# Optimization experiments

Measured on AMD Instinct MI355X. Metric: run time of the kernel, lower is better.

Reference implementation:

```python
import jax, jax.numpy as jnp
import numpy as np

B, S, D, U, L = 32, 8192, 64, 32, 2
VOCAB, E, NV = 10000, 500000, 50000


def _gru_dir(x, K, R, b_in, b_rec, reverse):
    # Keras GRU (v2 defaults, reset_after=True) over time axis.
    # x: [B, S, D_in]; K: [D_in, 3U]; R: [U, 3U]; b_in, b_rec: [3U]
    Bsz = x.shape[0]
    units = R.shape[0]

    def step(h, xt):
        mx = xt @ K + b_in          # [B, 3U]
        mi = h @ R + b_rec          # [B, 3U]
        xz, xr, xh = jnp.split(mx, 3, axis=-1)
        iz, ir, ih = jnp.split(mi, 3, axis=-1)
        z = jax.nn.sigmoid(xz + iz)
        r = jax.nn.sigmoid(xr + ir)
        hh = jnp.tanh(xh + r * ih)
        h = z * h + (1.0 - z) * hh
        return h, h

    h0 = jnp.zeros((Bsz, units), x.dtype)
    _, ys = jax.lax.scan(step, h0, jnp.swapaxes(x, 0, 1), reverse=reverse)
    return jnp.swapaxes(ys, 0, 1)  # [B, S, U]


def setup_inputs() -> dict:
    key = jax.random.key(0)
    ks = jax.random.split(key, 10)
    embedding_table = jax.random.normal(ks[0], (VOCAB, D), jnp.float32) * 0.02
    gru_kernels = jax.random.normal(ks[1], (L, 2, D, 3 * U), jnp.float32) * 0.1
    gru_rec_kernels = jax.random.normal(ks[2], (L, 2, U, 3 * U), jnp.float32) * 0.1
    gru_biases = jax.random.normal(ks[3], (L, 2, 2, 3 * U), jnp.float32) * 0.01
    linear_w = jax.random.normal(ks[4], (2 * U, 2 * U), jnp.float32) * 0.05
    embedding_gather_matrix = jax.random.randint(ks[5], (B, S), 0, VOCAB, jnp.int32)
    sequence_lengths = jax.random.randint(ks[6], (B,), 1, S + 1, jnp.int32)
    variable_bound_token_ids = jax.random.randint(ks[7], (E,), 0, B * S, jnp.int32)
    token_variable_ids = jax.random.randint(ks[8], (E,), 0, NV, jnp.int32)
    return {
        "embedding_table": embedding_table,
        "gru_kernels": gru_kernels,
        "gru_rec_kernels": gru_rec_kernels,
        "gru_biases": gru_biases,
        "linear_w": linear_w,
        "embedding_gather_matrix": embedding_gather_matrix,
        "sequence_lengths": sequence_lengths,
        "variable_bound_token_ids": variable_bound_token_ids,
        "token_variable_ids": token_variable_ids,
        "num_variables": NV,
    }


def reference(embedding_table, gru_kernels, gru_rec_kernels, gru_biases, linear_w,
              embedding_gather_matrix, sequence_lengths,
              variable_bound_token_ids, token_variable_ids, num_variables):
    # gather_nd: token id -> embedding, [B, S, D]
    x = embedding_table[embedding_gather_matrix]
    mask = (jnp.arange(S)[None, :, None] < sequence_lengths[:, None, None]).astype(x.dtype)

    def var_emb(cur):
        # gather per-occurrence token embeddings, unsorted_segment_mean per variable
        flat = cur.reshape(-1, cur.shape[-1])                      # [B*S, F]
        tgt = flat[variable_bound_token_ids]                       # [E, F]
        sums = jax.ops.segment_sum(tgt, token_variable_ids, num_segments=num_variables)
        cnt = jax.ops.segment_sum(jnp.ones((tgt.shape[0], 1), tgt.dtype),
                                  token_variable_ids, num_segments=num_variables)
        return sums / jnp.maximum(cnt, 1.0)                        # [NV, F]

    cur = x
    n_layers = gru_kernels.shape[0]
    for i in range(n_layers):
        cur = cur * mask
        f = _gru_dir(cur, gru_kernels[i, 0], gru_rec_kernels[i, 0],
                     gru_biases[i, 0, 0], gru_biases[i, 0, 1], reverse=False)
        b = _gru_dir(cur, gru_kernels[i, 1], gru_rec_kernels[i, 1],
                     gru_biases[i, 1, 0], gru_biases[i, 1, 1], reverse=True)
        cur = jnp.concatenate([f, b], axis=-1)                     # [B, S, 2U]
        if i < n_layers - 1:
            # consistency layer: scatter variable means back to tokens
            ve = var_emb(cur)                                      # [NV, 2U]
            per_tok = ve[token_variable_ids]                       # [E, 2U]
            upd = jnp.zeros((B * S, cur.shape[-1]), cur.dtype)
            upd = upd.at[variable_bound_token_ids].add(per_tok)    # scatter_nd (add dups)
            cur = cur + upd.reshape(B, S, -1)

    variable_embeddings = var_emb(cur)                             # [NV, 2U]
    classification_representation = variable_embeddings @ linear_w # dropout omitted (inference)
    return variable_embeddings, classification_representation
```

## Files before the change

### kernel.cpp

```cpp
#include <hip/hip_runtime.h>
#include <hip/hip_bf16.h>

typedef unsigned short ushort_t;
typedef unsigned int uint_t;

#define BB    32
#define SS    8192
#define DD    64
#define UU    32
#define GG    96
#define NEDGE 500000
#define NVAR  50000
#define VOCAB 10000

#define WT_KERN   0
#define WT_REC    24576
#define WT_BIAS   36864
#define WT_LW     37632
#define WT_TOTAL  41728

#define OFF_FLAG  0
#define OFF_WTS   16
#define OFF_SUMS  (OFF_WTS + WT_TOTAL)
#define OFF_CNT   (OFF_SUMS + NVAR*64)
#define OFF_CUR0  (OFF_CNT + NVAR)
#define OFF_CUR1  (OFF_CUR0 + BB*SS*DD)
#define WS_NEED_BYTES ((size_t)(OFF_CUR1 + BB*SS*DD) * 4)

__device__ __forceinline__ float bf2f(uint_t h) {
    union { uint_t u; float f; } v; v.u = h << 16; return v.f;
}
__device__ __forceinline__ float frcp(float x) { return __builtin_amdgcn_rcpf(x); }
__device__ __forceinline__ float sigm(float x) { return frcp(1.f + __expf(-x)); }
__device__ __forceinline__ float ftanh(float x) {
    return 1.f - 2.f * frcp(__expf(2.f * x) + 1.f);
}
__device__ __forceinline__ float fetchv(const void* p, int j, bool bf) {
    return bf ? bf2f(((const ushort_t*)p)[j]) : ((const float*)p)[j];
}

__global__ void k_sniff(const ushort_t* __restrict__ tab, int* __restrict__ flag) {
    if (threadIdx.x == 0 && blockIdx.x == 0) {
        int insane = 0;
        for (int i = 0; i < 128; i++) {
            float a = fabsf(bf2f(tab[i]));
            if (!(a <= 100.f)) insane++;
        }
        *flag = (insane <= 8) ? 1 : 0;
    }
}

__global__ __launch_bounds__(256) void k_cvt(
    const void* __restrict__ gk, const void* __restrict__ grk,
    const void* __restrict__ gb, const void* __restrict__ lw,
    const int* __restrict__ flag, float* __restrict__ wts)
{
    const bool bf = (*flag) != 0;
    int i = blockIdx.x * 256 + threadIdx.x;
    if (i < 24576)          wts[i] = fetchv(gk, i, bf);
    else if (i < 36864)     wts[i] = fetchv(grk, i - 24576, bf);
    else if (i < 37632)     wts[i] = fetchv(gb, i - 36864, bf);
    else if (i < WT_TOTAL)  wts[i] = fetchv(lw, i - 37632, bf);
}

template<int LAYER>
__global__ __launch_bounds__(192, 1) void k_gru(
    const void* __restrict__ table, const int* __restrict__ gm,
    const int* __restrict__ slen, const float* __restrict__ wts,
    const int* __restrict__ flagp,
    const float* __restrict__ curin,
    float* __restrict__ curout)
{
    const int bb = blockIdx.x >> 1, dir = blockIdx.x & 1;
    const int j = threadIdx.x;
    const bool bfin = (*flagp) != 0;
    const int myslen = slen[bb];

    const float* Km  = wts + WT_KERN + (size_t)(LAYER*2+dir)*(DD*GG);
    const float* R   = wts + WT_REC  + (size_t)(LAYER*2+dir)*(UU*GG);
    const float* bin = wts + WT_BIAS + (size_t)((LAYER*2+dir)*2 + 0)*GG;
    const float* brc = wts + WT_BIAS + (size_t)((LAYER*2+dir)*2 + 1)*GG;

    __shared__ __align__(16) float h_sh[UU];
    __shared__ float mi_sh[GG];
    __shared__ float mx_sh[3][GG];
    __shared__ float xs_sh[2][DD];

    float Rc[UU]; float bj = 0.f;
    float Kc[DD]; float bpj = 0.f;
    if (j < GG) {
#pragma unroll
        for (int k = 0; k < UU; k++) Rc[k] = R[k*GG + j];
        bj = brc[j];
    } else {
        const int pj = j - 96;
#pragma unroll
        for (int k = 0; k < DD; k++) Kc[k] = Km[k*GG + pj];
        bpj = bin[pj];
    }
    if (j < UU) h_sh[j] = 0.f;
    __syncthreads();

    const ushort_t* tab16 = (const ushort_t*)table;
    const float*    tab32 = (const float*)table;

    for (int su = 0; su <= SS + 2; su++) {
        float mi = bj, px = bpj, xv = 0.f;
        if (j < GG) {
            if (su >= 3) {
                float hr[UU];
#pragma unroll
                for (int kq = 0; kq < 8; kq++) {
                    float4 hv = reinterpret_cast<const float4*>(h_sh)[kq];
                    hr[kq*4]=hv.x; hr[kq*4+1]=hv.y; hr[kq*4+2]=hv.z; hr[kq*4+3]=hv.w;
                }
#pragma unroll
                for (int k = 0; k < UU; k++) mi = fmaf(hr[k], Rc[k], mi);
                mi_sh[j] = mi;
            }
        } else {
            if (su >= 1 && su <= SS) {
                const float* xs = xs_sh[(su-1)&1];
#pragma unroll
                for (int k = 0; k < DD; k++) px = fmaf(xs[k], Kc[k], px);
            }
            const int lk = j - 96;
            if (lk < DD && su < SS) {
                const int p3 = dir ? (SS-1-su) : su;
                if (p3 < myslen) {
                    if (LAYER == 0) {
                        const int idx = gm[(size_t)bb*SS + p3];
                        xv = bfin ? bf2f(tab16[(size_t)idx*DD + lk])
                                  : tab32[(size_t)idx*DD + lk];
                    } else {
                        xv = curin[((size_t)bb*SS + p3)*DD + lk];
                    }
                }
            }
        }
        __syncthreads();
        if (j < UU) {
            if (su >= 3) {
                const int s = su - 3;
                const int p = dir ? (SS-1-s) : s;
                const float* mrow = mx_sh[su % 3];
                const float z  = sigm(mrow[j]      + mi_sh[j]);
                const float r  = sigm(mrow[32 + j] + mi_sh[32 + j]);
                const float th = ftanh(mrow[64 + j] + r * mi_sh[64 + j]);
                const float hn = th + z * (h_sh[j] - th);
                h_sh[j] = hn;
                curout[((size_t)bb*SS + p)*DD + dir*UU + j] = hn;
            }
        } else if (j >= 96) {
            if (su >= 1 && su <= SS) mx_sh[(su-1) % 3][j-96] = px;
            const int lk = j - 96;
            if (lk < DD && su < SS) xs_sh[su & 1][lk] = xv;
        }
        __syncthreads();
    }
}

__global__ __launch_bounds__(256) void k_scatter_sum(
    const float* __restrict__ cur, const int* __restrict__ vbti,
    const int* __restrict__ tvi, float* __restrict__ sums, float* __restrict__ cnt)
{
    const int lane = threadIdx.x & 63;
    const int base = blockIdx.x * 4 + (threadIdx.x >> 6);
    for (int e = base; e < NEDGE; e += gridDim.x * 4) {
        const int tok = vbti[e];
        const int var = tvi[e];
        const float v = cur[(size_t)tok * 64 + lane];
        atomicAdd(&sums[(size_t)var * 64 + lane], v);
        if (lane == 0) atomicAdd(&cnt[var], 1.f);
    }
}

__global__ __launch_bounds__(256) void k_scatter_back(
    const float* __restrict__ means, const int* __restrict__ vbti,
    const int* __restrict__ tvi, float* __restrict__ cur)
{
    const int lane = threadIdx.x & 63;
    const int base = blockIdx.x * 4 + (threadIdx.x >> 6);
    for (int e = base; e < NEDGE; e += gridDim.x * 4) {
        const int tok = vbti[e];
        const int var = tvi[e];
        const float m = means[(size_t)var * 64 + lane];
        atomicAdd(&cur[(size_t)tok * 64 + lane], m);
    }
}

template<bool WRITE_OUT>
__global__ __launch_bounds__(256) void k_mean(
    float* __restrict__ sums, const float* __restrict__ cnt, float* __restrict__ out)
{
    const int i = blockIdx.x * 256 + threadIdx.x;
    if (i < NVAR * 64) {
        const float c = fmaxf(cnt[i >> 6], 1.f);
        const float v = sums[i] / c;
        sums[i] = v;
        if (WRITE_OUT) out[i] = v;
    }
}

__global__ __launch_bounds__(256) void k_class(
    const float* __restrict__ means, const float* __restrict__ w,
    float* __restrict__ out)
{
    __shared__ float Wl[64 * 64];
    for (int i = threadIdx.x; i < 4096; i += 256) Wl[i] = w[i];
    __syncthreads();
    const int gid = blockIdx.x * 256 + threadIdx.x;
    if (gid < NVAR * 64) {
        const int v = gid >> 6, jj = gid & 63;
        const float* mv = means + (size_t)v * 64;
        float acc = 0.f;
#pragma unroll
        for (int k = 0; k < 64; k++) acc = fmaf(mv[k], Wl[k * 64 + jj], acc);
        out[(size_t)NVAR * 64 + gid] = acc;
    }
}

__global__ void k_err(float* out, int prio) { out[0] = (float)(131072 << prio); }

extern "C" void kernel_launch(void* const* d_in, const int* in_sizes, int n_in,
                              void* d_out, int out_size, void* d_ws, size_t ws_size,
                              hipStream_t stream) {
    const void* table = d_in[0];
    const void* gk    = d_in[1];
    const void* grk   = d_in[2];
    const void* gb    = d_in[3];
    const void* lw    = d_in[4];
    const int* gm   = (const int*)d_in[5];
    const int* slen = (const int*)d_in[6];
    const int* vbti = (const int*)d_in[7];
    const int* tvi  = (const int*)d_in[8];
    float* out = (float*)d_out;

    if (ws_size < WS_NEED_BYTES) { k_err<<<1, 1, 0, stream>>>(out, 0); return; }
    if (n_in != 10)              { k_err<<<1, 1, 0, stream>>>(out, 1); return; }
    if (in_sizes[0] != VOCAB*DD || in_sizes[5] != BB*SS || in_sizes[6] != BB ||
        in_sizes[7] != NEDGE || in_sizes[8] != NEDGE) {
        k_err<<<1, 1, 0, stream>>>(out, 2); return;
    }
    if (out_size != 2*NVAR*64)   { k_err<<<1, 1, 0, stream>>>(out, 3); return; }

    float* W = (float*)d_ws;
    int*   flag = (int*)(W + OFF_FLAG);
    float* wts  = W + OFF_WTS;
    float* sums = W + OFF_SUMS;
    float* cnt  = W + OFF_CNT;
    float* cur0 = W + OFF_CUR0;
    float* cur1 = W + OFF_CUR1;

    k_sniff<<<1, 64, 0, stream>>>((const ushort_t*)table, flag);
    k_cvt<<<163, 256, 0, stream>>>(gk, grk, gb, lw, flag, wts);

    k_gru<0><<<64, 192, 0, stream>>>(table, gm, slen, wts, flag, nullptr, cur0);

    hipMemsetAsync(sums, 0, (size_t)(NVAR * 64 + NVAR) * sizeof(float), stream);
    k_scatter_sum<<<2048, 256, 0, stream>>>(cur0, vbti, tvi, sums, cnt);
    k_mean<false><<<12500, 256, 0, stream>>>(sums, cnt, nullptr);
    k_scatter_back<<<2048, 256, 0, stream>>>(sums, vbti, tvi, cur0);

    k_gru<1><<<64, 192, 0, stream>>>(table, gm, slen, wts, flag, cur0, cur1);

    hipMemsetAsync(sums, 0, (size_t)(NVAR * 64 + NVAR) * sizeof(float), stream);
    k_scatter_sum<<<2048, 256, 0, stream>>>(cur1, vbti, tvi, sums, cnt);
    k_mean<true><<<12500, 256, 0, stream>>>(sums, cnt, out);
    k_class<<<12500, 256, 0, stream>>>(sums, wts + WT_LW, out);
}
```

Measured before the change: 11.89 ms.

## Split GRU into chunked producer/consumer waves with wave-local recurrence

The GRU kernel is rebuilt as two 64-lane waves. One wave gathers inputs and computes the input projections for chunks of 16 timesteps into a double-buffered shared ring. The other wave runs the recurrence for a whole chunk, sharing the hidden state through shared memory and lane shuffles inside the wave, so there are no per-step block barriers. This targets the two __syncthreads per timestep on the serial critical path. The trade-off is one barrier per chunk, more register pressure, and reliance on wave-synchronous shared-memory ordering.

Result: no change. 11.86 ms (-0.3%).

```diff
diff --git a/kernel.cpp b/kernel.cpp
--- a/kernel.cpp
+++ b/kernel.cpp
@@ -13,6 +13,9 @@
 #define NVAR  50000
 #define VOCAB 10000
 
+#define CHUNK 16
+#define NCH   (SS / CHUNK)
+
 #define WT_KERN   0
 #define WT_REC    24576
 #define WT_BIAS   36864
@@ -64,7 +67,7 @@
 }
 
 template<int LAYER>
-__global__ __launch_bounds__(192, 1) void k_gru(
+__global__ __launch_bounds__(128, 1) void k_gru(
     const void* __restrict__ table, const int* __restrict__ gm,
     const int* __restrict__ slen, const float* __restrict__ wts,
     const int* __restrict__ flagp,
@@ -73,6 +76,8 @@
 {
     const int bb = blockIdx.x >> 1, dir = blockIdx.x & 1;
     const int j = threadIdx.x;
+    const int wv = j >> 6;
+    const int ln = j & 63;
     const bool bfin = (*flagp) != 0;
     const int myslen = slen[bb];
 
@@ -81,82 +86,114 @@
     const float* bin = wts + WT_BIAS + (size_t)((LAYER*2+dir)*2 + 0)*GG;
     const float* brc = wts + WT_BIAS + (size_t)((LAYER*2+dir)*2 + 1)*GG;
 
-    __shared__ __align__(16) float h_sh[UU];
-    __shared__ float mi_sh[GG];
-    __shared__ float mx_sh[3][GG];
-    __shared__ float xs_sh[2][DD];
-
-    float Rc[UU]; float bj = 0.f;
-    float Kc[DD]; float bpj = 0.f;
-    if (j < GG) {
-#pragma unroll
-        for (int k = 0; k < UU; k++) Rc[k] = R[k*GG + j];
-        bj = brc[j];
-    } else {
-        const int pj = j - 96;
-#pragma unroll
-        for (int k = 0; k < DD; k++) Kc[k] = Km[k*GG + pj];
-        bpj = bin[pj];
-    }
-    if (j < UU) h_sh[j] = 0.f;
-    __syncthreads();
+    __shared__ __align__(16) float ring[2][CHUNK][GG];
+    __shared__ __align__(16) float xbuf[CHUNK][DD];
+    __shared__ __align__(16) float hb[UU];
 
     const ushort_t* tab16 = (const ushort_t*)table;
     const float*    tab32 = (const float*)table;
 
-    for (int su = 0; su <= SS + 2; su++) {
-        float mi = bj, px = bpj, xv = 0.f;
-        if (j < GG) {
-            if (su >= 3) {
-                float hr[UU];
-#pragma unroll
-                for (int kq = 0; kq < 8; kq++) {
-                    float4 hv = reinterpret_cast<const float4*>(h_sh)[kq];
-                    hr[kq*4]=hv.x; hr[kq*4+1]=hv.y; hr[kq*4+2]=hv.z; hr[kq*4+3]=hv.w;
+    if (wv == 1) {
+        float K0[DD], K1[DD];
+        const float b0 = bin[ln];
+        const float b1 = (ln < 32) ? bin[64 + ln] : 0.f;
+#pragma unroll
+        for (int k = 0; k < DD; k++) {
+            K0[k] = Km[k*GG + ln];
+            K1[k] = (ln < 32) ? Km[k*GG + 64 + ln] : 0.f;
+        }
+        for (int c = 0; c <= NCH; c++) {
+            if (c < NCH) {
+                for (int stp = 0; stp < CHUNK; stp++) {
+                    const int s = c*CHUNK + stp;
+                    const int p = dir ? (SS-1-s) : s;
+                    float xv = 0.f;
+                    if (p < myslen) {
+                        if (LAYER == 0) {
+                            const int idx = gm[(size_t)bb*SS + p];
+                            xv = bfin ? bf2f(tab16[(size_t)idx*DD + ln])
+                                      : tab32[(size_t)idx*DD + ln];
+                        } else {
+                            xv = curin[((size_t)bb*SS + p)*DD + ln];
+                        }
+                    }
+                    xbuf[stp][ln] = xv;
                 }
-#pragma unroll
-                for (int k = 0; k < UU; k++) mi = fmaf(hr[k], Rc[k], mi);
-                mi_sh[j] = mi;
-            }
-        } else {
-            if (su >= 1 && su <= SS) {
-                const float* xs = xs_sh[(su-1)&1];
-#pragma unroll
-                for (int k = 0; k < DD; k++) px = fmaf(xs[k], Kc[k], px);
-            }
-            const int lk = j - 96;
-            if (lk < DD && su < SS) {
-                const int p3 = dir ? (SS-1-su) : su;
-                if (p3 < myslen) {
-                    if (LAYER == 0) {
-                        const int idx = gm[(size_t)bb*SS + p3];
-                        xv = bfin ? bf2f(tab16[(size_t)idx*DD + lk])
-                                  : tab32[(size_t)idx*DD + lk];
-                    } else {
-                        xv = curin[((size_t)bb*SS + p3)*DD + lk];
-                    }
+                float* rg = &ring[c & 1][0][0];
+                for (int stp = 0; stp < CHUNK; stp++) {
+                    float p0 = b0, p1 = b1;
+                    const float4* xr = reinterpret_cast<const float4*>(xbuf[stp]);
+#pragma unroll
+                    for (int q = 0; q < 16; q++) {
+                        const float4 xq = xr[q];
+                        p0 = fmaf(xq.x, K0[4*q+0], p0); p1 = fmaf(xq.x, K1[4*q+0], p1);
+                        p0 = fmaf(xq.y, K0[4*q+1], p0); p1 = fmaf(xq.y, K1[4*q+1], p1);
+                        p0 = fmaf(xq.z, K0[4*q+2], p0); p1 = fmaf(xq.z, K1[4*q+2], p1);
+                        p0 = fmaf(xq.w, K0[4*q+3], p0); p1 = fmaf(xq.w, K1[4*q+3], p1);
+                    }
+                    rg[stp*GG + ln] = p0;
+                    if (ln < 32) rg[stp*GG + 64 + ln] = p1;
                 }
             }
-        }
-        __syncthreads();
-        if (j < UU) {
-            if (su >= 3) {
-                const int s = su - 3;
-                const int p = dir ? (SS-1-s) : s;
-                const float* mrow = mx_sh[su % 3];
-                const float z  = sigm(mrow[j]      + mi_sh[j]);
-                const float r  = sigm(mrow[32 + j] + mi_sh[32 + j]);
-                const float th = ftanh(mrow[64 + j] + r * mi_sh[64 + j]);
-                const float hn = th + z * (h_sh[j] - th);
-                h_sh[j] = hn;
-                curout[((size_t)bb*SS + p)*DD + dir*UU + j] = hn;
+            __syncthreads();
+        }
+    } else {
+        const int u = ln & 31;
+        const int half = ln >> 5;
+        const int colA = half ? (64 + u) : u;
+        float wA[UU], wB[UU];
+        const float bA = brc[colA];
+        const float bB = half ? 0.f : brc[32 + u];
+#pragma unroll
+        for (int k = 0; k < UU; k++) {
+            wA[k] = R[k*GG + colA];
+            wB[k] = half ? 0.f : R[k*GG + 32 + u];
+        }
+        float h_own = 0.f;
+        float hreg[UU];
+#pragma unroll
+        for (int k = 0; k < UU; k++) hreg[k] = 0.f;
+
+        for (int c = 0; c <= NCH; c++) {
+            if (c > 0) {
+                const int c0 = c - 1;
+                const float* rg = &ring[c0 & 1][0][0];
+                for (int stp = 0; stp < CHUNK; stp++) {
+                    const int s = c0*CHUNK + stp;
+                    const int p = dir ? (SS-1-s) : s;
+                    const float mz = rg[stp*GG + u];
+                    const float mr = rg[stp*GG + 32 + u];
+                    const float mh = rg[stp*GG + 64 + u];
+                    float a = bA, cr = bB;
+#pragma unroll
+                    for (int k = 0; k < UU; k++) {
+                        a  = fmaf(hreg[k], wA[k], a);
+                        cr = fmaf(hreg[k], wB[k], cr);
+                    }
+                    const float ax = __shfl_xor(a, 32);
+                    const float cx = __shfl_xor(cr, 32);
+                    const float zd = half ? ax : a;
+                    const float rd = half ? cx : cr;
+                    const float hd = half ? a  : ax;
+                    const float z  = sigm(mz + zd);
+                    const float r  = sigm(mr + rd);
+                    const float th = ftanh(mh + r * hd);
+                    const float hn = th + z * (h_own - th);
+                    h_own = hn;
+                    if (half == 0) {
+                        hb[u] = hn;
+                        curout[((size_t)bb*SS + p)*DD + dir*UU + u] = hn;
+                    }
+#pragma unroll
+                    for (int q = 0; q < 8; q++) {
+                        const float4 hv = reinterpret_cast<const float4*>(hb)[q];
+                        hreg[4*q+0] = hv.x; hreg[4*q+1] = hv.y;
+                        hreg[4*q+2] = hv.z; hreg[4*q+3] = hv.w;
+                    }
+                }
             }
-        } else if (j >= 96) {
-            if (su >= 1 && su <= SS) mx_sh[(su-1) % 3][j-96] = px;
-            const int lk = j - 96;
-            if (lk < DD && su < SS) xs_sh[su & 1][lk] = xv;
-        }
-        __syncthreads();
+            __syncthreads();
+        }
     }
 }
 
@@ -255,14 +292,14 @@
     k_sniff<<<1, 64, 0, stream>>>((const ushort_t*)table, flag);
     k_cvt<<<163, 256, 0, stream>>>(gk, grk, gb, lw, flag, wts);
 
-    k_gru<0><<<64, 192, 0, stream>>>(table, gm, slen, wts, flag, nullptr, cur0);
+    k_gru<0><<<64, 128, 0, stream>>>(table, gm, slen, wts, flag, nullptr, cur0);
 
     hipMemsetAsync(sums, 0, (size_t)(NVAR * 64 + NVAR) * sizeof(float), stream);
     k_scatter_sum<<<2048, 256, 0, stream>>>(cur0, vbti, tvi, sums, cnt);
     k_mean<false><<<12500, 256, 0, stream>>>(sums, cnt, nullptr);
     k_scatter_back<<<2048, 256, 0, stream>>>(sums, vbti, tvi, cur0);
 
-    k_gru<1><<<64, 192, 0, stream>>>(table, gm, slen, wts, flag, cur0, cur1);
+    k_gru<1><<<64, 128, 0, stream>>>(table, gm, slen, wts, flag, cur0, cur1);
 
     hipMemsetAsync(sums, 0, (size_t)(NVAR * 64 + NVAR) * sizeof(float), stream);
     k_scatter_sum<<<2048, 256, 0, stream>>>(cur1, vbti, tvi, sums, cnt);
```
